# Optimization experiments

Measured on AMD Instinct MI355X. Metric: run time of the kernel, lower is better.

The kernel has to match this reference:

```python
import jax, jax.numpy as jnp
import numpy as np

B, K, E, L, H, ENS = 32768, 5, 16, 128, 3, 3

def setup_inputs() -> dict:
    key = jax.random.key(0)
    ks = jax.random.split(key, 16)
    w = lambda i, shape: (jax.random.normal(ks[i], shape, jnp.float32) * 0.05)
    return {
        "z": jax.random.normal(ks[0], (B, L), jnp.float32),
        "anchors": jax.random.normal(ks[1], (B, K, 2), jnp.float32),
        # anchor_embed MLP: Linear(2,E) -> ReLU -> Linear(E,E)
        "W1": w(2, (E, 2)), "b1": w(3, (E,)),
        "W2": w(4, (E, E)), "b2": w(5, (E,)),
        # LSTMCell(E, L): gates order i,f,g,o
        "W_ih": w(6, (4 * L, E)), "W_hh": w(7, (4 * L, L)),
        "b_ih": w(8, (4 * L,)), "b_hh": w(9, (4 * L,)),
        # progress head Linear(L,1)
        "Wp": w(10, (1, L)), "bp": w(11, (1,)),
        # risk ensemble: ENS stacked Linear(L,1)
        "Wr": w(12, (ENS, L)), "br": w(13, (ENS,)),
    }

def reference(z, anchors, W1, b1, W2, b2, W_ih, W_hh, b_ih, b_hh, Wp, bp, Wr, br):
    Bc, Kc, _ = anchors.shape
    # anchor embedding MLP (B,K,2) -> (B,K,E)
    emb = jnp.maximum(anchors @ W1.T + b1, 0.0) @ W2.T + b2
    inp = emb.reshape(Bc * Kc, -1)                      # (B*K, E)
    h = jnp.broadcast_to(z[:, None, :], (Bc, Kc, z.shape[-1])).reshape(Bc * Kc, -1)
    c = jnp.zeros_like(h)
    x_proj = inp @ W_ih.T + b_ih                        # input projection constant over steps
    for _ in range(H):  # fixed small rollout horizon
        gates = x_proj + h @ W_hh.T + b_hh              # (B*K, 4L)
        i_g, f_g, g_g, o_g = jnp.split(gates, 4, axis=-1)
        i_g = jax.nn.sigmoid(i_g)
        f_g = jax.nn.sigmoid(f_g)
        g_g = jnp.tanh(g_g)
        o_g = jax.nn.sigmoid(o_g)
        c = f_g * c + i_g * g_g
        h = o_g * jnp.tanh(c)
    h = h.reshape(Bc, Kc, -1)                           # (B,K,L)
    progress = (h @ Wp.T + bp)[..., 0]                  # (B,K)
    risks = jnp.einsum('bkl,el->ebk', h, Wr) + br[:, None, None]  # (ENS,B,K)
    risk_mean = risks.mean(axis=0)
    unc = jnp.var(jax.nn.sigmoid(risks), axis=0, ddof=1)  # torch .var is unbiased
    return risk_mean, progress, unc, risks
```

## Files before the change

kernel.cpp:

```cpp
#include <hip/hip_runtime.h>

#define BN 32768
#define KN 5
#define LN 128
#define HN 3
#define ROWS (BN*KN)
#define BK ROWS
#define MT 64
#define TILES (ROWS/MT)
#define WGS 512
#define TPW (TILES/WGS)
#define THREADS 512
#define ASTR 168
#define LOG2E 1.44269504089f

using bf16x8 = __attribute__((ext_vector_type(8))) __bf16;
using bf16x2 = __attribute__((ext_vector_type(2))) __bf16;
using f32x4  = __attribute__((ext_vector_type(4))) float;
using u16x8  = __attribute__((ext_vector_type(8))) unsigned short;

__device__ inline unsigned short f2bf(float x) {
    union { float f; unsigned u; } v; v.f = x;
    unsigned r = v.u + 0x7FFFu + ((v.u >> 16) & 1u);
    return (unsigned short)(r >> 16);
}
#if __has_builtin(__builtin_amdgcn_cvt_pk_bf16_f32)
__device__ inline unsigned short f2bf_fast(float x) {
    union { bf16x2 v; unsigned short us[2]; } u;
    u.v = __builtin_amdgcn_cvt_pk_bf16_f32(x, x);
    return u.us[0];
}
#else
__device__ inline unsigned short f2bf_fast(float x) { return f2bf(x); }
#endif
__device__ inline float bf2f(unsigned short b) {
    union { unsigned u; float f; } v; v.u = ((unsigned)b) << 16; return v.f;
}
__device__ inline float sigm(float x) {
    return __builtin_amdgcn_rcpf(1.0f + __builtin_amdgcn_exp2f(-LOG2E * x));
}
__device__ inline f32x4 splat4(float x) { f32x4 r; r[0]=x; r[1]=x; r[2]=x; r[3]=x; return r; }

__global__ __launch_bounds__(THREADS, 2)
void wahead_kernel(const float* __restrict__ z,   const float* __restrict__ anchors,
                   const float* __restrict__ W1,  const float* __restrict__ b1,
                   const float* __restrict__ W2,  const float* __restrict__ b2,
                   const float* __restrict__ Wih, const float* __restrict__ Whh,
                   const float* __restrict__ bih, const float* __restrict__ bhh,
                   const float* __restrict__ Wp,  const float* __restrict__ bp,
                   const float* __restrict__ Wr,  const float* __restrict__ br,
                   float* __restrict__ out)
{
    __shared__ unsigned short sA[2 * MT * ASTR];
    __shared__ float sW1[32], sb1[16], sW2[16 * 17], sb2[16], sWp[128], sWr[384];

    const int tid  = threadIdx.x;
    const int wv   = tid >> 6;
    const int lane = tid & 63;
    const int quad = lane >> 4;
    const int cc   = lane & 15;

    if (tid < 32)  sW1[tid] = W1[tid];
    if (tid < 16)  { sb1[tid] = b1[tid]; sb2[tid] = b2[tid]; }
    if (tid < 256) sW2[(tid >> 4) * 17 + (tid & 15)] = W2[tid];
    if (tid < 128) sWp[tid] = Wp[tid];
    if (tid < 384) sWr[tid] = Wr[tid];

    bf16x8 Bf[4][5];
    float  biasv[4];
    #pragma unroll
    for (int t = 0; t < 4; ++t) {
        const float sc = (t == 2) ? (2.0f * LOG2E) : (-LOG2E);
        const int n = t * 128 + wv * 16 + cc;
        biasv[t] = sc * (bih[n] + bhh[n]);
        #pragma unroll
        for (int kt = 0; kt < 5; ++kt) {
            const int k0 = kt * 32 + quad * 8;
            float v[8];
            if (k0 < 16) {
                const float4 p0 = *reinterpret_cast<const float4*>(Wih + n * 16 + k0);
                const float4 p1 = *reinterpret_cast<const float4*>(Wih + n * 16 + k0 + 4);
                v[0]=p0.x; v[1]=p0.y; v[2]=p0.z; v[3]=p0.w;
                v[4]=p1.x; v[5]=p1.y; v[6]=p1.z; v[7]=p1.w;
            } else if (k0 < 144) {
                const float4 p0 = *reinterpret_cast<const float4*>(Whh + n * 128 + (k0 - 16));
                const float4 p1 = *reinterpret_cast<const float4*>(Whh + n * 128 + (k0 - 16) + 4);
                v[0]=p0.x; v[1]=p0.y; v[2]=p0.z; v[3]=p0.w;
                v[4]=p1.x; v[5]=p1.y; v[6]=p1.z; v[7]=p1.w;
            } else {
                #pragma unroll
                for (int j = 0; j < 8; ++j) v[j] = 0.0f;
            }
            union { bf16x8 bv; unsigned short us[8]; } pk;
            #pragma unroll
            for (int j = 0; j < 8; ++j) pk.us[j] = f2bf(sc * v[j]);
            Bf[t][kt] = pk.bv;
        }
    }

    const float bpv = bp[0];
    const float br0 = br[0], br1 = br[1], br2 = br[2];

    __syncthreads();

    const int erow = tid >> 3;
    const int esub = tid & 7;

    #pragma unroll 1
    for (int ti = 0; ti < TPW; ++ti) {
        const int tile = blockIdx.x * TPW + ti;
        const int r0g  = tile * MT;

        {
            const int gr = r0g + erow;
            const float ax = anchors[gr * 2], ay = anchors[gr * 2 + 1];
            const int e0 = esub * 2;
            float a0 = sb2[e0], a1 = sb2[e0 + 1];
            #pragma unroll
            for (int hh = 0; hh < 16; ++hh) {
                float pre = fmaf(sW1[hh * 2], ax, fmaf(sW1[hh * 2 + 1], ay, sb1[hh]));
                pre = fmaxf(pre, 0.0f);
                a0 = fmaf(pre, sW2[e0 * 17 + hh], a0);
                a1 = fmaf(pre, sW2[(e0 + 1) * 17 + hh], a1);
            }
            const unsigned short b0 = f2bf(a0), b1v = f2bf(a1);
            #pragma unroll
            for (int bufi = 0; bufi < 2; ++bufi) {
                unsigned short* row = &sA[bufi * MT * ASTR + erow * ASTR];
                row[e0]       = b0;  row[e0 + 1]       = b1v;
                row[144 + e0] = 0;   row[144 + e0 + 1] = 0;
            }
            const unsigned b_idx = (unsigned)gr / 5u;
            const float4* zp = reinterpret_cast<const float4*>(z + (size_t)b_idx * 128 + esub * 16);
            const float4 z0 = zp[0], z1 = zp[1], z2 = zp[2], z3 = zp[3];
            union { u16x8 v; unsigned short us[8]; } w0, w1;
            w0.us[0]=f2bf(z0.x); w0.us[1]=f2bf(z0.y); w0.us[2]=f2bf(z0.z); w0.us[3]=f2bf(z0.w);
            w0.us[4]=f2bf(z1.x); w0.us[5]=f2bf(z1.y); w0.us[6]=f2bf(z1.z); w0.us[7]=f2bf(z1.w);
            w1.us[0]=f2bf(z2.x); w1.us[1]=f2bf(z2.y); w1.us[2]=f2bf(z2.z); w1.us[3]=f2bf(z2.w);
            w1.us[4]=f2bf(z3.x); w1.us[5]=f2bf(z3.y); w1.us[6]=f2bf(z3.z); w1.us[7]=f2bf(z3.w);
            unsigned short* hrow = &sA[erow * ASTR + 16 + esub * 16];
            *reinterpret_cast<u16x8*>(hrow)     = w0.v;
            *reinterpret_cast<u16x8*>(hrow + 8) = w1.v;
        }

        float cst[16];
        #pragma unroll
        for (int e = 0; e < 16; ++e) cst[e] = 0.0f;

        #pragma unroll
        for (int s = 0; s < HN; ++s) {
            const int cur = s & 1;
            const int nxt = cur ^ 1;
            __syncthreads();

            f32x4 acc[4][4];
            #pragma unroll
            for (int mt = 0; mt < 4; ++mt)
                #pragma unroll
                for (int t = 0; t < 4; ++t)
                    acc[mt][t] = splat4(biasv[t]);

            bf16x8 af[2][5];
            #pragma unroll
            for (int kt = 0; kt < 5; ++kt)
                af[0][kt] = *reinterpret_cast<const bf16x8*>(
                    &sA[cur * MT * ASTR + cc * ASTR + kt * 32 + quad * 8]);
            #pragma unroll
            for (int mt = 0; mt < 4; ++mt) {
                const int pb = mt & 1;
                if (mt < 3) {
                    #pragma unroll
                    for (int kt = 0; kt < 5; ++kt)
                        af[pb ^ 1][kt] = *reinterpret_cast<const bf16x8*>(
                            &sA[cur * MT * ASTR + ((mt + 1) * 16 + cc) * ASTR + kt * 32 + quad * 8]);
                }
                #pragma unroll
                for (int kt = 0; kt < 5; ++kt)
                    #pragma unroll
                    for (int t = 0; t < 4; ++t)
                        acc[mt][t] = __builtin_amdgcn_mfma_f32_16x16x32_bf16(
                            af[pb][kt], Bf[t][kt], acc[mt][t], 0, 0, 0);
            }

            const int lcol = wv * 16 + cc;
            #pragma unroll
            for (int e = 0; e < 16; ++e) {
                const int mt = e >> 2, r = e & 3;
                const float Ei = __builtin_amdgcn_exp2f(acc[mt][0][r]);
                const float Ef = __builtin_amdgcn_exp2f(acc[mt][1][r]);
                const float Eg = __builtin_amdgcn_exp2f(acc[mt][2][r]);
                const float Eo = __builtin_amdgcn_exp2f(acc[mt][3][r]);
                const float t1  = (1.0f + Ei) * (1.0f + Eg);
                const float ef1 = 1.0f + Ef;
                const float t3  = (Eg - 1.0f) * ef1;
                const float num = fmaf(cst[e], t1, t3);
                const float cn  = num * __builtin_amdgcn_rcpf(t1 * ef1);
                cst[e] = cn;
                const float Ec = __builtin_amdgcn_exp2f(2.0f * LOG2E * cn);
                const float hn = (Ec - 1.0f) *
                    __builtin_amdgcn_rcpf((1.0f + Eo) * (1.0f + Ec));
                const int m = mt * 16 + quad * 4 + r;
                sA[nxt * MT * ASTR + m * ASTR + 16 + lcol] = f2bf_fast(hn);
            }
        }

        __syncthreads();

        {
            const int row = tid >> 3;
            const int j   = tid & 7;
            const unsigned short* hrow = &sA[1 * MT * ASTR + row * ASTR + 16 + j * 16];
            const u16x8 h0 = *reinterpret_cast<const u16x8*>(hrow);
            const u16x8 h1 = *reinterpret_cast<const u16x8*>(hrow + 8);
            float p = 0.f, q0 = 0.f, q1 = 0.f, q2 = 0.f;
            #pragma unroll
            for (int u = 0; u < 16; ++u) {
                const int l = j * 16 + u;
                const float hv = bf2f(u < 8 ? h0[u] : h1[u - 8]);
                p  = fmaf(hv, sWp[l], p);
                q0 = fmaf(hv, sWr[l], q0);
                q1 = fmaf(hv, sWr[128 + l], q1);
                q2 = fmaf(hv, sWr[256 + l], q2);
            }
            #pragma unroll
            for (int m = 1; m < 8; m <<= 1) {
                p  += __shfl_xor(p,  m, 64);
                q0 += __shfl_xor(q0, m, 64);
                q1 += __shfl_xor(q1, m, 64);
                q2 += __shfl_xor(q2, m, 64);
            }
            if (j == 0) {
                const int gr = r0g + row;
                const float prog  = p + bpv;
                const float rr0 = q0 + br0, rr1 = q1 + br1, rr2 = q2 + br2;
                const float rmean = (rr0 + rr1 + rr2) * (1.0f / 3.0f);
                const float s0 = sigm(rr0), s1 = sigm(rr1), s2 = sigm(rr2);
                const float sm = (s0 + s1 + s2) * (1.0f / 3.0f);
                const float d0 = s0 - sm, d1 = s1 - sm, d2 = s2 - sm;
                const float unc = (d0 * d0 + d1 * d1 + d2 * d2) * 0.5f;
                out[gr]          = rmean;
                out[BK + gr]     = prog;
                out[2 * BK + gr] = unc;
                out[3 * BK + gr] = rr0;
                out[4 * BK + gr] = rr1;
                out[5 * BK + gr] = rr2;
            }
        }
    }
}

extern "C" void kernel_launch(void* const* d_in, const int* in_sizes, int n_in,
                              void* d_out, int out_size, void* d_ws, size_t ws_size,
                              hipStream_t stream) {
    const float* z       = (const float*)d_in[0];
    const float* anchors = (const float*)d_in[1];
    const float* W1      = (const float*)d_in[2];
    const float* b1      = (const float*)d_in[3];
    const float* W2      = (const float*)d_in[4];
    const float* b2      = (const float*)d_in[5];
    const float* Wih     = (const float*)d_in[6];
    const float* Whh     = (const float*)d_in[7];
    const float* bih     = (const float*)d_in[8];
    const float* bhh     = (const float*)d_in[9];
    const float* Wp      = (const float*)d_in[10];
    const float* bp      = (const float*)d_in[11];
    const float* Wr      = (const float*)d_in[12];
    const float* br      = (const float*)d_in[13];

    hipLaunchKernelGGL(wahead_kernel, dim3(WGS), dim3(THREADS), 0, stream,
                       z, anchors, W1, b1, W2, b2, Wih, Whh, bih, bhh,
                       Wp, bp, Wr, br, (float*)d_out);
}
```

Measured before the change: 214.1 us.

## Prefetch next tile inputs and interleave LSTM pointwise with MFMA issue

Loads the next tile's anchors and z rows into registers during the last rollout step, so global-load latency overlaps with compute instead of stalling at the start of each tile. The gate nonlinearities for each 16-row M-subtile now run right after that subtile's MFMAs finish, while later subtiles' MFMAs are still in flight. Transcendental VALU work then overlaps with matrix-core work. The cost is higher register pressure from the prefetched float4s and from live accumulators, which could cause spills at two waves per SIMD.

```diff
diff --git a/kernel.cpp b/kernel.cpp
--- a/kernel.cpp
+++ b/kernel.cpp
@@ -41,6 +41,27 @@
 }
 __device__ inline f32x4 splat4(float x) { f32x4 r; r[0]=x; r[1]=x; r[2]=x; r[3]=x; return r; }
 
+#define POINTWISE(MTI) do {                                                        \
+    _Pragma("unroll")                                                              \
+    for (int r_ = 0; r_ < 4; ++r_) {                                               \
+        const float Ei = __builtin_amdgcn_exp2f(acc[MTI][0][r_]);       \
+        const float Ef = __builtin_amdgcn_exp2f(acc[MTI][1][r_]);       \
+        const float Eg = __builtin_amdgcn_exp2f(acc[MTI][2][r_]);       \
+        const float Eo = __builtin_amdgcn_exp2f(acc[MTI][3][r_]);       \
+        const float t1  = (1.0f + Ei) * (1.0f + Eg);                               \
+        const float ef1 = 1.0f + Ef;                                               \
+        const float t3  = (Eg - 1.0f) * ef1;                                       \
+        const float num = fmaf(cst[(MTI)*4 + r_], t1, t3);                         \
+        const float cn  = num * __builtin_amdgcn_rcpf(t1 * ef1);                   \
+        cst[(MTI)*4 + r_] = cn;                                                    \
+        const float Ec = __builtin_amdgcn_exp2f(2.0f * LOG2E * cn);                \
+        const float hn = (Ec - 1.0f) *                                             \
+            __builtin_amdgcn_rcpf((1.0f + Eo) * (1.0f + Ec));                      \
+        sA[nxt * MT * ASTR + ((MTI)*16 + quad*4 + r_) * ASTR + 16 + lcol] =        \
+            f2bf_fast(hn);                                                         \
+    }                                                                              \
+} while (0)
+
 __global__ __launch_bounds__(THREADS, 2)
 void wahead_kernel(const float* __restrict__ z,   const float* __restrict__ anchors,
                    const float* __restrict__ W1,  const float* __restrict__ b1,
@@ -59,6 +80,7 @@
     const int lane = tid & 63;
     const int quad = lane >> 4;
     const int cc   = lane & 15;
+    const int lcol = wv * 16 + cc;
 
     if (tid < 32)  sW1[tid] = W1[tid];
     if (tid < 16)  { sb1[tid] = b1[tid]; sb2[tid] = b2[tid]; }
@@ -106,14 +128,24 @@
     const int erow = tid >> 3;
     const int esub = tid & 7;
 
+    float  pax, pay;
+    float4 pz0, pz1, pz2, pz3;
+    {
+        const int gr = blockIdx.x * TPW * MT + erow;
+        const float2 an = *reinterpret_cast<const float2*>(anchors + gr * 2);
+        pax = an.x; pay = an.y;
+        const unsigned b_idx = (unsigned)gr / 5u;
+        const float4* zp = reinterpret_cast<const float4*>(z + (size_t)b_idx * 128 + esub * 16);
+        pz0 = zp[0]; pz1 = zp[1]; pz2 = zp[2]; pz3 = zp[3];
+    }
+
     #pragma unroll 1
     for (int ti = 0; ti < TPW; ++ti) {
         const int tile = blockIdx.x * TPW + ti;
         const int r0g  = tile * MT;
 
         {
-            const int gr = r0g + erow;
-            const float ax = anchors[gr * 2], ay = anchors[gr * 2 + 1];
+            const float ax = pax, ay = pay;
             const int e0 = esub * 2;
             float a0 = sb2[e0], a1 = sb2[e0 + 1];
             #pragma unroll
@@ -130,14 +162,11 @@
                 row[e0]       = b0;  row[e0 + 1]       = b1v;
                 row[144 + e0] = 0;   row[144 + e0 + 1] = 0;
             }
-            const unsigned b_idx = (unsigned)gr / 5u;
-            const float4* zp = reinterpret_cast<const float4*>(z + (size_t)b_idx * 128 + esub * 16);
-            const float4 z0 = zp[0], z1 = zp[1], z2 = zp[2], z3 = zp[3];
             union { u16x8 v; unsigned short us[8]; } w0, w1;
-            w0.us[0]=f2bf(z0.x); w0.us[1]=f2bf(z0.y); w0.us[2]=f2bf(z0.z); w0.us[3]=f2bf(z0.w);
-            w0.us[4]=f2bf(z1.x); w0.us[5]=f2bf(z1.y); w0.us[6]=f2bf(z1.z); w0.us[7]=f2bf(z1.w);
-            w1.us[0]=f2bf(z2.x); w1.us[1]=f2bf(z2.y); w1.us[2]=f2bf(z2.z); w1.us[3]=f2bf(z2.w);
-            w1.us[4]=f2bf(z3.x); w1.us[5]=f2bf(z3.y); w1.us[6]=f2bf(z3.z); w1.us[7]=f2bf(z3.w);
+            w0.us[0]=f2bf(pz0.x); w0.us[1]=f2bf(pz0.y); w0.us[2]=f2bf(pz0.z); w0.us[3]=f2bf(pz0.w);
+            w0.us[4]=f2bf(pz1.x); w0.us[5]=f2bf(pz1.y); w0.us[6]=f2bf(pz1.z); w0.us[7]=f2bf(pz1.w);
+            w1.us[0]=f2bf(pz2.x); w1.us[1]=f2bf(pz2.y); w1.us[2]=f2bf(pz2.z); w1.us[3]=f2bf(pz2.w);
+            w1.us[4]=f2bf(pz3.x); w1.us[5]=f2bf(pz3.y); w1.us[6]=f2bf(pz3.z); w1.us[7]=f2bf(pz3.w);
             unsigned short* hrow = &sA[erow * ASTR + 16 + esub * 16];
             *reinterpret_cast<u16x8*>(hrow)     = w0.v;
             *reinterpret_cast<u16x8*>(hrow + 8) = w1.v;
@@ -152,6 +181,15 @@
             const int cur = s & 1;
             const int nxt = cur ^ 1;
             __syncthreads();
+
+            if (s == HN - 1 && ti + 1 < TPW) {
+                const int gr = (r0g + MT) + erow;
+                const float2 an = *reinterpret_cast<const float2*>(anchors + gr * 2);
+                pax = an.x; pay = an.y;
+                const unsigned b_idx = (unsigned)gr / 5u;
+                const float4* zp = reinterpret_cast<const float4*>(z + (size_t)b_idx * 128 + esub * 16);
+                pz0 = zp[0]; pz1 = zp[1]; pz2 = zp[2]; pz3 = zp[3];
+            }
 
             f32x4 acc[4][4];
             #pragma unroll
@@ -180,28 +218,11 @@
                     for (int t = 0; t < 4; ++t)
                         acc[mt][t] = __builtin_amdgcn_mfma_f32_16x16x32_bf16(
                             af[pb][kt], Bf[t][kt], acc[mt][t], 0, 0, 0);
-            }
-
-            const int lcol = wv * 16 + cc;
-            #pragma unroll
-            for (int e = 0; e < 16; ++e) {
-                const int mt = e >> 2, r = e & 3;
-                const float Ei = __builtin_amdgcn_exp2f(acc[mt][0][r]);
-                const float Ef = __builtin_amdgcn_exp2f(acc[mt][1][r]);
-                const float Eg = __builtin_amdgcn_exp2f(acc[mt][2][r]);
-                const float Eo = __builtin_amdgcn_exp2f(acc[mt][3][r]);
-                const float t1  = (1.0f + Ei) * (1.0f + Eg);
-                const float ef1 = 1.0f + Ef;
-                const float t3  = (Eg - 1.0f) * ef1;
-                const float num = fmaf(cst[e], t1, t3);
-                const float cn  = num * __builtin_amdgcn_rcpf(t1 * ef1);
-                cst[e] = cn;
-                const float Ec = __builtin_amdgcn_exp2f(2.0f * LOG2E * cn);
-                const float hn = (Ec - 1.0f) *
-                    __builtin_amdgcn_rcpf((1.0f + Eo) * (1.0f + Ec));
-                const int m = mt * 16 + quad * 4 + r;
-                sA[nxt * MT * ASTR + m * ASTR + 16 + lcol] = f2bf_fast(hn);
-            }
+                if (mt == 1) POINTWISE(0);
+                else if (mt == 2) POINTWISE(1);
+                else if (mt == 3) POINTWISE(2);
+            }
+            POINTWISE(3);
         }
 
         __syncthreads();
```

New measurement: 213.7 us. No clear change (-0.2%).

## Split LSTM gate columns across two wave halves with LDS gate exchange

Applied to the files above, without the earlier changes.

Doubles the workgroup to 1024 threads and halves the grid. Each wave now holds only two of the four gate weight fragments, which cuts VGPR pressure. The two wave halves compute complementary gate pairs for both row halves and swap one half of their results through a new LDS gate buffer, so each wave applies the cell update to 32 rows. The embedding moves to its own small LDS buffer, and the h layout drops the embedded offset. This adds an extra barrier and LDS round-trip per step in exchange for lower register use and possibly higher occupancy.

```diff
diff --git a/kernel.cpp b/kernel.cpp
--- a/kernel.cpp
+++ b/kernel.cpp
@@ -8,10 +8,12 @@
 #define BK ROWS
 #define MT 64
 #define TILES (ROWS/MT)
-#define WGS 512
+#define WGS 256
 #define TPW (TILES/WGS)
-#define THREADS 512
-#define ASTR 168
+#define THREADS 1024
+#define HSTR 152
+#define ESTR 24
+#define GSTR 36
 #define LOG2E 1.44269504089f
 
 using bf16x8 = __attribute__((ext_vector_type(8))) __bf16;
@@ -41,7 +43,7 @@
 }
 __device__ inline f32x4 splat4(float x) { f32x4 r; r[0]=x; r[1]=x; r[2]=x; r[3]=x; return r; }
 
-__global__ __launch_bounds__(THREADS, 2)
+__global__ __launch_bounds__(THREADS, 4)
 void wahead_kernel(const float* __restrict__ z,   const float* __restrict__ anchors,
                    const float* __restrict__ W1,  const float* __restrict__ b1,
                    const float* __restrict__ W2,  const float* __restrict__ b2,
@@ -51,14 +53,19 @@
                    const float* __restrict__ Wr,  const float* __restrict__ br,
                    float* __restrict__ out)
 {
-    __shared__ unsigned short sA[2 * MT * ASTR];
+    __shared__ __align__(16) unsigned short sH[2 * MT * HSTR];
+    __shared__ __align__(16) unsigned short sEmb[MT * ESTR];
+    __shared__ __align__(16) float sG[8 * 2 * 2 * 16 * GSTR];
     __shared__ float sW1[32], sb1[16], sW2[16 * 17], sb2[16], sWp[128], sWr[384];
 
     const int tid  = threadIdx.x;
-    const int wv   = tid >> 6;
+    const int wvid = tid >> 6;
+    const int cg   = wvid & 7;
+    const int wh   = wvid >> 3;
     const int lane = tid & 63;
     const int quad = lane >> 4;
     const int cc   = lane & 15;
+    const int lcol = cg * 16 + cc;
 
     if (tid < 32)  sW1[tid] = W1[tid];
     if (tid < 16)  { sb1[tid] = b1[tid]; sb2[tid] = b2[tid]; }
@@ -66,13 +73,21 @@
     if (tid < 128) sWp[tid] = Wp[tid];
     if (tid < 384) sWr[tid] = Wr[tid];
 
-    bf16x8 Bf[4][5];
-    float  biasv[4];
+    {
+        const int bnum = tid >> 9;
+        const int rr   = (tid >> 3) & 63;
+        const int c0   = 128 + (tid & 7) * 2;
+        *reinterpret_cast<unsigned*>(&sH[bnum * MT * HSTR + rr * HSTR + c0]) = 0u;
+    }
+
+    bf16x8 Bf[2][5];
+    float  biasv[2];
     #pragma unroll
-    for (int t = 0; t < 4; ++t) {
+    for (int g = 0; g < 2; ++g) {
+        const int t = wh * 2 + g;
         const float sc = (t == 2) ? (2.0f * LOG2E) : (-LOG2E);
-        const int n = t * 128 + wv * 16 + cc;
-        biasv[t] = sc * (bih[n] + bhh[n]);
+        const int n = t * 128 + lcol;
+        biasv[g] = sc * (bih[n] + bhh[n]);
         #pragma unroll
         for (int kt = 0; kt < 5; ++kt) {
             const int k0 = kt * 32 + quad * 8;
@@ -94,7 +109,7 @@
             union { bf16x8 bv; unsigned short us[8]; } pk;
             #pragma unroll
             for (int j = 0; j < 8; ++j) pk.us[j] = f2bf(sc * v[j]);
-            Bf[t][kt] = pk.bv;
+            Bf[g][kt] = pk.bv;
         }
     }
 
@@ -103,8 +118,8 @@
 
     __syncthreads();
 
-    const int erow = tid >> 3;
-    const int esub = tid & 7;
+    const int erow = tid >> 4;
+    const int esub = tid & 15;
 
     #pragma unroll 1
     for (int ti = 0; ti < TPW; ++ti) {
@@ -113,39 +128,27 @@
 
         {
             const int gr = r0g + erow;
-            const float ax = anchors[gr * 2], ay = anchors[gr * 2 + 1];
-            const int e0 = esub * 2;
-            float a0 = sb2[e0], a1 = sb2[e0 + 1];
+            const float2 an = *reinterpret_cast<const float2*>(anchors + gr * 2);
+            float a0 = sb2[esub];
             #pragma unroll
             for (int hh = 0; hh < 16; ++hh) {
-                float pre = fmaf(sW1[hh * 2], ax, fmaf(sW1[hh * 2 + 1], ay, sb1[hh]));
+                float pre = fmaf(sW1[hh * 2], an.x, fmaf(sW1[hh * 2 + 1], an.y, sb1[hh]));
                 pre = fmaxf(pre, 0.0f);
-                a0 = fmaf(pre, sW2[e0 * 17 + hh], a0);
-                a1 = fmaf(pre, sW2[(e0 + 1) * 17 + hh], a1);
-            }
-            const unsigned short b0 = f2bf(a0), b1v = f2bf(a1);
-            #pragma unroll
-            for (int bufi = 0; bufi < 2; ++bufi) {
-                unsigned short* row = &sA[bufi * MT * ASTR + erow * ASTR];
-                row[e0]       = b0;  row[e0 + 1]       = b1v;
-                row[144 + e0] = 0;   row[144 + e0 + 1] = 0;
-            }
+                a0 = fmaf(pre, sW2[esub * 17 + hh], a0);
+            }
+            sEmb[erow * ESTR + esub] = f2bf(a0);
             const unsigned b_idx = (unsigned)gr / 5u;
-            const float4* zp = reinterpret_cast<const float4*>(z + (size_t)b_idx * 128 + esub * 16);
-            const float4 z0 = zp[0], z1 = zp[1], z2 = zp[2], z3 = zp[3];
-            union { u16x8 v; unsigned short us[8]; } w0, w1;
+            const float4* zp = reinterpret_cast<const float4*>(z + (size_t)b_idx * 128 + esub * 8);
+            const float4 z0 = zp[0], z1 = zp[1];
+            union { u16x8 v; unsigned short us[8]; } w0;
             w0.us[0]=f2bf(z0.x); w0.us[1]=f2bf(z0.y); w0.us[2]=f2bf(z0.z); w0.us[3]=f2bf(z0.w);
             w0.us[4]=f2bf(z1.x); w0.us[5]=f2bf(z1.y); w0.us[6]=f2bf(z1.z); w0.us[7]=f2bf(z1.w);
-            w1.us[0]=f2bf(z2.x); w1.us[1]=f2bf(z2.y); w1.us[2]=f2bf(z2.z); w1.us[3]=f2bf(z2.w);
-            w1.us[4]=f2bf(z3.x); w1.us[5]=f2bf(z3.y); w1.us[6]=f2bf(z3.z); w1.us[7]=f2bf(z3.w);
-            unsigned short* hrow = &sA[erow * ASTR + 16 + esub * 16];
-            *reinterpret_cast<u16x8*>(hrow)     = w0.v;
-            *reinterpret_cast<u16x8*>(hrow + 8) = w1.v;
+            *reinterpret_cast<u16x8*>(&sH[erow * HSTR + esub * 8]) = w0.v;
         }
 
-        float cst[16];
+        float cst[8];
         #pragma unroll
-        for (int e = 0; e < 16; ++e) cst[e] = 0.0f;
+        for (int e = 0; e < 8; ++e) cst[e] = 0.0f;
 
         #pragma unroll
         for (int s = 0; s < HN; ++s) {
@@ -153,85 +156,119 @@
             const int nxt = cur ^ 1;
             __syncthreads();
 
-            f32x4 acc[4][4];
-            #pragma unroll
-            for (int mt = 0; mt < 4; ++mt)
-                #pragma unroll
-                for (int t = 0; t < 4; ++t)
-                    acc[mt][t] = splat4(biasv[t]);
-
-            bf16x8 af[2][5];
-            #pragma unroll
-            for (int kt = 0; kt < 5; ++kt)
-                af[0][kt] = *reinterpret_cast<const bf16x8*>(
-                    &sA[cur * MT * ASTR + cc * ASTR + kt * 32 + quad * 8]);
-            #pragma unroll
-            for (int mt = 0; mt < 4; ++mt) {
-                const int pb = mt & 1;
-                if (mt < 3) {
+            f32x4 acc[2][2][2];
+            #pragma unroll
+            for (int os = 0; os < 2; ++os)
+                #pragma unroll
+                for (int mo = 0; mo < 2; ++mo)
                     #pragma unroll
-                    for (int kt = 0; kt < 5; ++kt)
-                        af[pb ^ 1][kt] = *reinterpret_cast<const bf16x8*>(
-                            &sA[cur * MT * ASTR + ((mt + 1) * 16 + cc) * ASTR + kt * 32 + quad * 8]);
+                    for (int g = 0; g < 2; ++g)
+                        acc[os][mo][g] = splat4(biasv[g]);
+
+            const unsigned short* sHc = &sH[cur * MT * HSTR];
+
+            #pragma unroll
+            for (int osi = 0; osi < 2; ++osi) {
+                const int os = 1 - osi;
+                const int hb = os ? (wh ^ 1) : wh;
+                #pragma unroll
+                for (int mo = 0; mo < 2; ++mo) {
+                    const int arow = (hb * 2 + mo) * 16 + cc;
+                    const unsigned short* hr = &sHc[arow * HSTR];
+                    const unsigned short* a0p = (quad < 2)
+                        ? &sEmb[arow * ESTR + quad * 8]
+                        : &hr[(quad - 2) * 8];
+                    const bf16x8 af0 = *reinterpret_cast<const bf16x8*>(a0p);
+                    const bf16x8 af1 = *reinterpret_cast<const bf16x8*>(&hr[16  + quad * 8]);
+                    const bf16x8 af2 = *reinterpret_cast<const bf16x8*>(&hr[48  + quad * 8]);
+                    const bf16x8 af3 = *reinterpret_cast<const bf16x8*>(&hr[80  + quad * 8]);
+                    const bf16x8 af4 = *reinterpret_cast<const bf16x8*>(&hr[112 + quad * 8]);
+                    #pragma unroll
+                    for (int g = 0; g < 2; ++g) {
+                        acc[os][mo][g] = __builtin_amdgcn_mfma_f32_16x16x32_bf16(af0, Bf[g][0], acc[os][mo][g], 0, 0, 0);
+                        acc[os][mo][g] = __builtin_amdgcn_mfma_f32_16x16x32_bf16(af1, Bf[g][1], acc[os][mo][g], 0, 0, 0);
+                        acc[os][mo][g] = __builtin_amdgcn_mfma_f32_16x16x32_bf16(af2, Bf[g][2], acc[os][mo][g], 0, 0, 0);
+                        acc[os][mo][g] = __builtin_amdgcn_mfma_f32_16x16x32_bf16(af3, Bf[g][3], acc[os][mo][g], 0, 0, 0);
+                        acc[os][mo][g] = __builtin_amdgcn_mfma_f32_16x16x32_bf16(af4, Bf[g][4], acc[os][mo][g], 0, 0, 0);
+                    }
                 }
-                #pragma unroll
-                for (int kt = 0; kt < 5; ++kt)
+                if (os == 1) {
                     #pragma unroll
-                    for (int t = 0; t < 4; ++t)
-                        acc[mt][t] = __builtin_amdgcn_mfma_f32_16x16x32_bf16(
-                            af[pb][kt], Bf[t][kt], acc[mt][t], 0, 0, 0);
-            }
-
-            const int lcol = wv * 16 + cc;
-            #pragma unroll
-            for (int e = 0; e < 16; ++e) {
-                const int mt = e >> 2, r = e & 3;
-                const float Ei = __builtin_amdgcn_exp2f(acc[mt][0][r]);
-                const float Ef = __builtin_amdgcn_exp2f(acc[mt][1][r]);
-                const float Eg = __builtin_amdgcn_exp2f(acc[mt][2][r]);
-                const float Eo = __builtin_amdgcn_exp2f(acc[mt][3][r]);
-                const float t1  = (1.0f + Ei) * (1.0f + Eg);
-                const float ef1 = 1.0f + Ef;
-                const float t3  = (Eg - 1.0f) * ef1;
-                const float num = fmaf(cst[e], t1, t3);
-                const float cn  = num * __builtin_amdgcn_rcpf(t1 * ef1);
-                cst[e] = cn;
-                const float Ec = __builtin_amdgcn_exp2f(2.0f * LOG2E * cn);
-                const float hn = (Ec - 1.0f) *
-                    __builtin_amdgcn_rcpf((1.0f + Eo) * (1.0f + Ec));
-                const int m = mt * 16 + quad * 4 + r;
-                sA[nxt * MT * ASTR + m * ASTR + 16 + lcol] = f2bf_fast(hn);
+                    for (int mo = 0; mo < 2; ++mo)
+                        #pragma unroll
+                        for (int g = 0; g < 2; ++g)
+                            *reinterpret_cast<f32x4*>(
+                                &sG[(((cg * 2 + wh) * 2 + g) * 16 + cc) * GSTR + mo * 16 + quad * 4]) =
+                                acc[1][mo][g];
+                }
+            }
+
+            __syncthreads();
+
+            f32x4 og[2][2];
+            #pragma unroll
+            for (int mo = 0; mo < 2; ++mo)
+                #pragma unroll
+                for (int g = 0; g < 2; ++g)
+                    og[mo][g] = *reinterpret_cast<const f32x4*>(
+                        &sG[(((cg * 2 + (wh ^ 1)) * 2 + g) * 16 + cc) * GSTR + mo * 16 + quad * 4]);
+
+            unsigned short* sHn = &sH[nxt * MT * HSTR];
+            #pragma unroll
+            for (int mo = 0; mo < 2; ++mo) {
+                const f32x4 vi = wh ? og[mo][0]     : acc[0][mo][0];
+                const f32x4 vf = wh ? og[mo][1]     : acc[0][mo][1];
+                const f32x4 vg = wh ? acc[0][mo][0] : og[mo][0];
+                const f32x4 vo = wh ? acc[0][mo][1] : og[mo][1];
+                #pragma unroll
+                for (int r = 0; r < 4; ++r) {
+                    const int e = mo * 4 + r;
+                    const float Ei = __builtin_amdgcn_exp2f(vi[r]);
+                    const float Ef = __builtin_amdgcn_exp2f(vf[r]);
+                    const float Eg = __builtin_amdgcn_exp2f(vg[r]);
+                    const float Eo = __builtin_amdgcn_exp2f(vo[r]);
+                    const float t1  = (1.0f + Ei) * (1.0f + Eg);
+                    const float ef1 = 1.0f + Ef;
+                    const float t3  = (Eg - 1.0f) * ef1;
+                    const float num = fmaf(cst[e], t1, t3);
+                    const float cn  = num * __builtin_amdgcn_rcpf(t1 * ef1);
+                    cst[e] = cn;
+                    const float Ec = __builtin_amdgcn_exp2f(2.0f * LOG2E * cn);
+                    const float hn = (Ec - 1.0f) *
+                        __builtin_amdgcn_rcpf((1.0f + Eo) * (1.0f + Ec));
+                    const int row = wh * 32 + mo * 16 + quad * 4 + r;
+                    sHn[row * HSTR + lcol] = f2bf_fast(hn);
+                }
             }
         }
 
         __syncthreads();
 
         {
-            const int row = tid >> 3;
-            const int j   = tid & 7;
-            const unsigned short* hrow = &sA[1 * MT * ASTR + row * ASTR + 16 + j * 16];
-            const u16x8 h0 = *reinterpret_cast<const u16x8*>(hrow);
-            const u16x8 h1 = *reinterpret_cast<const u16x8*>(hrow + 8);
-            float p = 0.f, q0 = 0.f, q1 = 0.f, q2 = 0.f;
-            #pragma unroll
-            for (int u = 0; u < 16; ++u) {
-                const int l = j * 16 + u;
-                const float hv = bf2f(u < 8 ? h0[u] : h1[u - 8]);
-                p  = fmaf(hv, sWp[l], p);
+            const int row = tid >> 4;
+            const int j   = tid & 15;
+            const u16x8 h0 = *reinterpret_cast<const u16x8*>(
+                &sH[1 * MT * HSTR + row * HSTR + j * 8]);
+            float pp = 0.f, q0 = 0.f, q1 = 0.f, q2 = 0.f;
+            #pragma unroll
+            for (int u = 0; u < 8; ++u) {
+                const int l = j * 8 + u;
+                const float hv = bf2f(h0[u]);
+                pp = fmaf(hv, sWp[l], pp);
                 q0 = fmaf(hv, sWr[l], q0);
                 q1 = fmaf(hv, sWr[128 + l], q1);
                 q2 = fmaf(hv, sWr[256 + l], q2);
             }
             #pragma unroll
-            for (int m = 1; m < 8; m <<= 1) {
-                p  += __shfl_xor(p,  m, 64);
+            for (int m = 1; m < 16; m <<= 1) {
+                pp += __shfl_xor(pp, m, 64);
                 q0 += __shfl_xor(q0, m, 64);
                 q1 += __shfl_xor(q1, m, 64);
                 q2 += __shfl_xor(q2, m, 64);
             }
             if (j == 0) {
                 const int gr = r0g + row;
-                const float prog  = p + bpv;
+                const float prog  = pp + bpv;
                 const float rr0 = q0 + br0, rr1 = q1 + br1, rr2 = q2 + br2;
                 const float rmean = (rr0 + rr1 + rr2) * (1.0f / 3.0f);
                 const float s0 = sigm(rr0), s1 = sigm(rr1), s2 = sigm(rr2);
```

Measured after the change: 240.6 us. 1.12x slower.
